# Kernel optimization log

Measured on AMD Instinct MI355X. Metric: run time of the kernel, lower is better.

The kernel has to match this reference:

```python
import jax, jax.numpy as jnp
import numpy as np

B, N, K, E, D, L, LM = 4, 5000, 4, 80000, 512, 6, 3
EPS_MSG = 1e-7   # GENConv message eps
EPS_SM = 1e-16   # PyG scatter-softmax eps
EPS_BN = 1e-5    # BatchNorm eps (eval: running mean=0, var=1)
EPS_LN = 1e-5


def setup_inputs() -> dict:
    key = jax.random.key(0)
    ks = jax.random.split(key, 12)
    s = 0.04  # weight scale for stability
    return {
        "x_idx": jax.random.randint(ks[0], (B, N, K), 0, 25, dtype=jnp.int32),
        "edge_index": jax.random.randint(ks[1], (2, E), 0, N, dtype=jnp.int32),
        "edge_weight": jax.random.uniform(ks[2], (E,), dtype=jnp.float32),
        "node_emb": jax.random.normal(ks[3], (25, D), dtype=jnp.float32),
        "W1": jax.random.normal(ks[4], (L, D, 2 * D), dtype=jnp.float32) * s,
        "b1": jnp.zeros((L, 2 * D), jnp.float32),
        "g1": jnp.ones((L, 2 * D), jnp.float32),
        "be1": jnp.zeros((L, 2 * D), jnp.float32),
        "W2": jax.random.normal(ks[5], (L, 2 * D, D), dtype=jnp.float32) * s,
        "b2": jnp.zeros((L, D), jnp.float32),
        "ln_g": jnp.ones((D,), jnp.float32),
        "ln_b": jnp.zeros((D,), jnp.float32),
        "Wm": jax.random.normal(ks[6], (LM, D, D), dtype=jnp.float32) * s,
        "bm": jnp.zeros((LM, D), jnp.float32),
        "Wout": jax.random.normal(ks[7], (D, 1), dtype=jnp.float32) * s,
        "bout": jnp.zeros((1,), jnp.float32),
    }


def _gen_conv(x, src, dst, edge_weight, W1, b1, g1, be1, W2, b2):
    # x: [B,N,D]; GENConv(aggr='softmax', t=1, num_layers=2, norm='batch' in eval)
    x_j = x[:, src, :]                                            # [B,E,D] gather
    msg = jax.nn.relu(x_j + edge_weight[None, :, None]) + EPS_MSG # [B,E,D]

    def seg_softmax_agg(m):  # m: [E,D] -> [N,D]
        mx = jax.ops.segment_max(m, dst, num_segments=N)          # [N,D]
        ex = jnp.exp(m - mx[dst])
        den = jax.ops.segment_sum(ex, dst, num_segments=N)
        alpha = ex / (den[dst] + EPS_SM)
        return jax.ops.segment_sum(m * alpha, dst, num_segments=N)

    agg = jax.vmap(seg_softmax_agg)(msg)                          # [B,N,D]
    out = agg + x                                                 # residual with x_dst
    h = out @ W1 + b1                                             # [B,N,2D]
    h = h / jnp.sqrt(1.0 + EPS_BN) * g1 + be1                     # BN eval (mean=0, var=1)
    h = jax.nn.relu(h)
    return h @ W2 + b2                                            # [B,N,D]


def reference(x_idx, edge_index, edge_weight, node_emb, W1, b1, g1, be1, W2, b2,
              ln_g, ln_b, Wm, bm, Wout, bout):
    src, dst = edge_index[0], edge_index[1]
    x = node_emb[x_idx].sum(axis=2)                               # [B,N,D]
    for l in range(W1.shape[0]):
        x = _gen_conv(x, src, dst, edge_weight,
                      W1[l], b1[l], g1[l], be1[l], W2[l], b2[l])
        x = jax.nn.relu(x)                                        # EncoderLayer relu (dropout=id in eval)
    mu = x.mean(axis=-1, keepdims=True)
    var = jnp.mean(jnp.square(x - mu), axis=-1, keepdims=True)
    h = (x - mu) * jax.lax.rsqrt(var + EPS_LN) * ln_g + ln_b      # LayerNorm
    for l in range(Wm.shape[0]):
        h = jax.nn.gelu(h @ Wm[l] + bm[l], approximate=False)
    out = h @ Wout + bout                                         # [B,N,1]
    return out.mean(axis=1)                                       # [B,1]
```

## Files before the change

kernel.cpp:

```cpp
#include <hip/hip_runtime.h>
#include <hip/hip_fp16.h>

#define BB 4
#define NN 5000
#define KK 4
#define EE 80000
#define DD 512
#define LL 6
#define LMM 3

typedef _Float16 f16x8 __attribute__((ext_vector_type(8)));
typedef _Float16 f16x4 __attribute__((ext_vector_type(4)));
typedef _Float16 f16x2 __attribute__((ext_vector_type(2)));
typedef float f32x4 __attribute__((ext_vector_type(4)));

__device__ __forceinline__ void async_copy16(_Float16* lds, const _Float16* g) {
    __builtin_amdgcn_global_load_lds((const __attribute__((address_space(1))) void*)g,
                                     (__attribute__((address_space(3))) void*)lds,
                                     16, 0, 0);
}

__global__ void zero_int2(int* a, int* b, int n) {
    int i = blockIdx.x * blockDim.x + threadIdx.x;
    if (i < n) { a[i] = 0; b[i] = 0; }
}

__global__ void count_deg(const int* __restrict__ dst, int* __restrict__ deg) {
    int e = blockIdx.x * blockDim.x + threadIdx.x;
    if (e < EE) atomicAdd(&deg[dst[e]], 1);
}

__global__ __launch_bounds__(1024) void scan_off(const int* __restrict__ deg, int* __restrict__ off) {
    __shared__ int s[1024];
    const int n = NN, tot = NN + 1;
    const int per = (tot + 1023) / 1024;
    int tid = threadIdx.x;
    int start = tid * per;
    int loc[8];
    int sum = 0;
    for (int i = 0; i < per; i++) {
        int idx = start + i;
        int v = (idx < n) ? deg[idx] : 0;
        loc[i] = sum; sum += v;
    }
    s[tid] = sum; __syncthreads();
    for (int o = 1; o < 1024; o <<= 1) {
        int v = (tid >= o) ? s[tid - o] : 0;
        __syncthreads();
        s[tid] += v;
        __syncthreads();
    }
    int base = (tid > 0) ? s[tid - 1] : 0;
    for (int i = 0; i < per; i++) {
        int idx = start + i;
        if (idx < tot) off[idx] = base + loc[i];
    }
}

__global__ void scatter_edges(const int* __restrict__ src, const int* __restrict__ dst,
                              const float* __restrict__ ew, const int* __restrict__ off,
                              int* __restrict__ cursor, int* __restrict__ srcs, float* __restrict__ wss) {
    int e = blockIdx.x * blockDim.x + threadIdx.x;
    if (e >= EE) return;
    int d = dst[e];
    int p = atomicAdd(&cursor[d], 1);
    int idx = off[d] + p;
    srcs[idx] = src[e];
    wss[idx] = ew[e];
}

__global__ __launch_bounds__(256) void embed_kernel(const int* __restrict__ x_idx,
                                                    const float* __restrict__ emb,
                                                    _Float16* __restrict__ x) {
    int row = blockIdx.x;
    int d = threadIdx.x * 2;
    int4 iv = *reinterpret_cast<const int4*>(x_idx + (size_t)row * 4);
    float2 a = *reinterpret_cast<const float2*>(emb + (size_t)iv.x * DD + d);
    float2 b = *reinterpret_cast<const float2*>(emb + (size_t)iv.y * DD + d);
    float2 c = *reinterpret_cast<const float2*>(emb + (size_t)iv.z * DD + d);
    float2 e = *reinterpret_cast<const float2*>(emb + (size_t)iv.w * DD + d);
    f16x2 v;
    v[0] = (_Float16)(a.x + b.x + c.x + e.x);
    v[1] = (_Float16)(a.y + b.y + c.y + e.y);
    *reinterpret_cast<f16x2*>(x + (size_t)row * DD + d) = v;
}

__global__ __launch_bounds__(128) void conv_kernel(const _Float16* __restrict__ x,
                                                   const int* __restrict__ srcs,
                                                   const float* __restrict__ wss,
                                                   const int* __restrict__ off,
                                                   _Float16* __restrict__ t) {
    int bh = blockIdx.x;
    int b = bh >> 1, h = bh & 1;
    int wave = threadIdx.x >> 6, lane = threadIdx.x & 63;
    int n = blockIdx.y * 2 + wave;
    const _Float16* xb = x + (size_t)b * NN * DD + h * (DD / 2);
    int e0 = off[n], e1 = off[n + 1];
    __shared__ int   ss[2][64];
    __shared__ float sw[2][64];
    int d0 = lane * 4;
    float S[4] = {0.f, 0.f, 0.f, 0.f};
    float Z[4] = {0.f, 0.f, 0.f, 0.f};
    for (int base = e0; base < e1; base += 64) {
        int cnt = min(64, e1 - base);
        if (lane < cnt) { ss[wave][lane] = srcs[base + lane]; sw[wave][lane] = wss[base + lane]; }
        for (int j = 0; j < cnt; j++) {
            f16x4 xv = *reinterpret_cast<const f16x4*>(xb + (size_t)ss[wave][j] * DD + d0);
            float w = sw[wave][j];
#pragma unroll
            for (int q = 0; q < 4; q++) {
                float m = fmaxf((float)xv[q] + w, 0.f);
                float p = __expf(m);
                S[q] += p;
                Z[q] = fmaf(m, p, Z[q]);
            }
        }
    }
    f16x4 xn = *reinterpret_cast<const f16x4*>(xb + (size_t)n * DD + d0);
    f16x4 o;
#pragma unroll
    for (int q = 0; q < 4; q++) {
        float agg = (e1 > e0) ? (Z[q] / (S[q] + 1e-16f) + 1e-7f) : 0.f;
        o[q] = (_Float16)(agg + (float)xn[q]);
    }
    *reinterpret_cast<f16x4*>(t + ((size_t)b * NN + n) * DD + h * (DD / 2) + d0) = o;
}

__global__ void transpose_f32_f16(const float* __restrict__ W, _Float16* __restrict__ Wt,
                                  int K, int Nc) {
    __shared__ float tile[32][33];
    size_t loff = (size_t)blockIdx.z * K * Nc;
    int n0 = blockIdx.x * 32, k0 = blockIdx.y * 32;
    int tx = threadIdx.x, ty = threadIdx.y;
    for (int i = 0; i < 32; i += 8)
        tile[ty + i][tx] = W[loff + (size_t)(k0 + ty + i) * Nc + n0 + tx];
    __syncthreads();
    for (int i = 0; i < 32; i += 8)
        Wt[loff + (size_t)(n0 + ty + i) * K + k0 + tx] = (_Float16)tile[tx][ty + i];
}

template <int MODE>
__global__ __launch_bounds__(256) void gemm_kernel(const _Float16* __restrict__ A,
                                                   const _Float16* __restrict__ Bt,
                                                   const float* __restrict__ bias,
                                                   const float* __restrict__ g,
                                                   const float* __restrict__ be,
                                                   _Float16* __restrict__ Cout,
                                                   int M, int N, int K, int nt) {
    constexpr int BM = 128, BN = 128, BK = 32;
    constexpr int BUF = (BM + BN) * BK;
    __shared__ __align__(16) _Float16 smem[2 * BUF];
    int tid = threadIdx.x;
    int bid = blockIdx.x;
    int xcd = bid & 7, gidx = bid >> 3;
    int m0 = (xcd + 8 * (gidx / nt)) * BM;
    int n0 = (gidx % nt) * BN;
    int lane = tid & 63, wave = tid >> 6;
    int wm = (wave & 1) * 64, wn = (wave >> 1) * 64;
    int l16 = lane & 15, quad = lane >> 4;
    int r0 = tid >> 2, r1 = r0 + 64;
    int c0s = ((tid & 3) ^ (r0 & 3)) * 8;
    int c1s = ((tid & 3) ^ (r1 & 3)) * 8;
    const _Float16* pa0 = A + (size_t)min(m0 + r0, M - 1) * K + c0s;
    const _Float16* pa1 = A + (size_t)min(m0 + r1, M - 1) * K + c1s;
    const _Float16* pb0 = Bt + (size_t)(n0 + r0) * K + c0s;
    const _Float16* pb1 = Bt + (size_t)(n0 + r1) * K + c1s;
    int la0 = tid * 8, la1 = (tid + 256) * 8;
    int lb0 = BM * BK + la0, lb1 = BM * BK + la1;

    f32x4 acc[4][4] = {};
    async_copy16(smem + la0, pa0);
    async_copy16(smem + la1, pa1);
    async_copy16(smem + lb0, pb0);
    async_copy16(smem + lb1, pb1);
    int buf = 0;
    int qa = (quad ^ (l16 & 3)) * 8;
    for (int k0 = 0; k0 < K; k0 += BK, buf ^= BUF) {
        __syncthreads();
        int kn = k0 + BK;
        int nb = buf ^ BUF;
        if (kn < K) {
            async_copy16(smem + nb + la0, pa0 + kn);
            async_copy16(smem + nb + la1, pa1 + kn);
            async_copy16(smem + nb + lb0, pb0 + kn);
            async_copy16(smem + nb + lb1, pb1 + kn);
        }
        f16x8 af[4], bf[4];
#pragma unroll
        for (int i = 0; i < 4; i++)
            af[i] = *reinterpret_cast<const f16x8*>(&smem[buf + (wm + i * 16 + l16) * BK + qa]);
#pragma unroll
        for (int j = 0; j < 4; j++)
            bf[j] = *reinterpret_cast<const f16x8*>(&smem[buf + BM * BK + (wn + j * 16 + l16) * BK + qa]);
#pragma unroll
        for (int i = 0; i < 4; i++)
#pragma unroll
            for (int j = 0; j < 4; j++)
                acc[i][j] = __builtin_amdgcn_mfma_f32_16x16x32_f16(af[i], bf[j], acc[i][j], 0, 0, 0);
    }
    __syncthreads();
    const float invs = rsqrtf(1.0f + 1e-5f);
    _Float16* Ct = smem;
#pragma unroll
    for (int p = 0; p < 2; p++) {
        if ((wave >> 1) == p) {
#pragma unroll
            for (int i = 0; i < 4; i++) {
#pragma unroll
                for (int j = 0; j < 4; j++) {
                    int col = n0 + wn + j * 16 + l16;
#pragma unroll
                    for (int r = 0; r < 4; r++) {
                        float v = acc[i][j][r] + bias[col];
                        if (MODE == 0) {
                            v = fmaxf(v * (g[col] * invs) + be[col], 0.f);
                        } else if (MODE == 1) {
                            v = fmaxf(v, 0.f);
                        } else {
                            v = 0.5f * v * (1.0f + erff(v * 0.70710678118654752f));
                        }
                        Ct[(wm + i * 16 + quad * 4 + r) * 64 + j * 16 + l16] = (_Float16)v;
                    }
                }
            }
        }
        __syncthreads();
#pragma unroll
        for (int k = 0; k < 4; k++) {
            int ch = tid + 256 * k;
            int row = ch >> 3, cc = (ch & 7) * 8;
            int grow = m0 + row;
            if (grow < M)
                *reinterpret_cast<f16x8*>(Cout + (size_t)grow * N + n0 + p * 64 + cc) =
                    *reinterpret_cast<const f16x8*>(&Ct[row * 64 + cc]);
        }
        __syncthreads();
    }
}

__device__ __forceinline__ float block_sum_256(float v, volatile float* sbuf) {
    __syncthreads();
    for (int s = 32; s; s >>= 1) v += __shfl_down(v, s);
    int wv = threadIdx.x >> 6, ln = threadIdx.x & 63;
    if (ln == 0) sbuf[wv] = v;
    __syncthreads();
    if (threadIdx.x == 0) sbuf[4] = sbuf[0] + sbuf[1] + sbuf[2] + sbuf[3];
    __syncthreads();
    return sbuf[4];
}

__global__ __launch_bounds__(256) void ln_kernel(const _Float16* __restrict__ x,
                                                 const float* __restrict__ lg,
                                                 const float* __restrict__ lb,
                                                 _Float16* __restrict__ t) {
    __shared__ float sbuf[5];
    size_t row = blockIdx.x;
    int d = threadIdx.x * 2;
    f16x2 xv = *reinterpret_cast<const f16x2*>(x + row * DD + d);
    float v0 = (float)xv[0], v1 = (float)xv[1];
    float mu = block_sum_256(v0 + v1, sbuf) * (1.0f / DD);
    float d0 = v0 - mu, d1 = v1 - mu;
    float var = block_sum_256(d0 * d0 + d1 * d1, sbuf) * (1.0f / DD);
    float rs = rsqrtf(var + 1e-5f);
    f16x2 o;
    o[0] = (_Float16)(d0 * rs * lg[d] + lb[d]);
    o[1] = (_Float16)(d1 * rs * lg[d + 1] + lb[d + 1]);
    *reinterpret_cast<f16x2*>(t + row * DD + d) = o;
}

__global__ void init_out(float* out, const float* __restrict__ bout) {
    if (threadIdx.x < BB) out[threadIdx.x] = bout[0];
}

__global__ __launch_bounds__(256) void final_reduce(const _Float16* __restrict__ h,
                                                    const float* __restrict__ wout,
                                                    float* __restrict__ out) {
    int b = blockIdx.y;
    const _Float16* hb = h + (size_t)b * NN * DD;
    int lane = threadIdx.x & 63, wave = threadIdx.x >> 6;
    float wv[8];
#pragma unroll
    for (int j = 0; j < 8; j++) wv[j] = wout[lane * 8 + j];
    float acc = 0.f;
    for (int n = blockIdx.x * 4 + wave; n < NN; n += gridDim.x * 4) {
        f16x8 hv = *reinterpret_cast<const f16x8*>(hb + (size_t)n * DD + lane * 8);
#pragma unroll
        for (int j = 0; j < 8; j++) acc += (float)hv[j] * wv[j];
    }
    for (int s = 32; s; s >>= 1) acc += __shfl_down(acc, s);
    __shared__ float sb[4];
    if (lane == 0) sb[wave] = acc;
    __syncthreads();
    if (threadIdx.x == 0) atomicAdd(&out[b], (sb[0] + sb[1] + sb[2] + sb[3]) * (1.0f / NN));
}

extern "C" void kernel_launch(void* const* d_in, const int* in_sizes, int n_in,
                              void* d_out, int out_size, void* d_ws, size_t ws_size,
                              hipStream_t stream) {
    const int*   x_idx = (const int*)d_in[0];
    const int*   eidx  = (const int*)d_in[1];
    const float* ew    = (const float*)d_in[2];
    const float* emb   = (const float*)d_in[3];
    const float* W1    = (const float*)d_in[4];
    const float* b1    = (const float*)d_in[5];
    const float* g1    = (const float*)d_in[6];
    const float* be1   = (const float*)d_in[7];
    const float* W2    = (const float*)d_in[8];
    const float* b2    = (const float*)d_in[9];
    const float* lng   = (const float*)d_in[10];
    const float* lnb   = (const float*)d_in[11];
    const float* Wm    = (const float*)d_in[12];
    const float* bm    = (const float*)d_in[13];
    const float* Wout  = (const float*)d_in[14];
    const float* bout  = (const float*)d_in[15];
    float* out = (float*)d_out;

    char* w = (char*)d_ws;
    size_t o = 0;
    auto alloc = [&](size_t bytes) -> void* {
        void* p = w + o;
        o = (o + bytes + 255) & ~(size_t)255;
        return p;
    };
    _Float16*  x    = (_Float16*)alloc((size_t)BB * NN * DD * 2);
    _Float16*  t    = (_Float16*)alloc((size_t)BB * NN * DD * 2);
    _Float16*  h    = (_Float16*)alloc((size_t)BB * NN * 2 * DD * 2);
    _Float16*  W1t  = (_Float16*)alloc((size_t)LL * 2 * DD * DD * 2);
    _Float16*  W2t  = (_Float16*)alloc((size_t)LL * DD * 2 * DD * 2);
    _Float16*  Wmt  = (_Float16*)alloc((size_t)LMM * DD * DD * 2);
    int*    deg    = (int*)alloc((size_t)NN * 4);
    int*    offs   = (int*)alloc((size_t)(NN + 1) * 4);
    int*    cursor = (int*)alloc((size_t)NN * 4);
    int*    srcs   = (int*)alloc((size_t)EE * 4);
    float*  wss    = (float*)alloc((size_t)EE * 4);

    const int* src = eidx;
    const int* dst = eidx + EE;

    zero_int2<<<(NN + 255) / 256, 256, 0, stream>>>(deg, cursor, NN);
    count_deg<<<(EE + 255) / 256, 256, 0, stream>>>(dst, deg);
    scan_off<<<1, 1024, 0, stream>>>(deg, offs);
    scatter_edges<<<(EE + 255) / 256, 256, 0, stream>>>(src, dst, ew, offs, cursor, srcs, wss);
    embed_kernel<<<BB * NN, 256, 0, stream>>>(x_idx, emb, x);

    transpose_f32_f16<<<dim3(2 * DD / 32, DD / 32, LL), dim3(32, 8), 0, stream>>>(W1, W1t, DD, 2 * DD);
    transpose_f32_f16<<<dim3(DD / 32, 2 * DD / 32, LL), dim3(32, 8), 0, stream>>>(W2, W2t, 2 * DD, DD);
    transpose_f32_f16<<<dim3(DD / 32, DD / 32, LMM), dim3(32, 8), 0, stream>>>(Wm, Wmt, DD, DD);

    const int M = BB * NN;
    const int mt8 = ((M + 127) / 128 + 7) & ~7;
    for (int l = 0; l < LL; l++) {
        conv_kernel<<<dim3(2 * BB, NN / 2), 128, 0, stream>>>(x, srcs, wss, offs, t);
        gemm_kernel<0><<<mt8 * 8, 256, 0, stream>>>(
            t, W1t + (size_t)l * 2 * DD * DD, b1 + (size_t)l * 2 * DD,
            g1 + (size_t)l * 2 * DD, be1 + (size_t)l * 2 * DD, h, M, 2 * DD, DD, 8);
        gemm_kernel<1><<<mt8 * 4, 256, 0, stream>>>(
            h, W2t + (size_t)l * DD * 2 * DD, b2 + (size_t)l * DD,
            nullptr, nullptr, x, M, DD, 2 * DD, 4);
    }
    ln_kernel<<<M, 256, 0, stream>>>(x, lng, lnb, t);
    gemm_kernel<2><<<mt8 * 4, 256, 0, stream>>>(
        t, Wmt, bm, nullptr, nullptr, h, M, DD, DD, 4);
    gemm_kernel<2><<<mt8 * 4, 256, 0, stream>>>(
        h, Wmt + (size_t)DD * DD, bm + DD, nullptr, nullptr, t, M, DD, DD, 4);
    gemm_kernel<2><<<mt8 * 4, 256, 0, stream>>>(
        t, Wmt + (size_t)2 * DD * DD, bm + 2 * DD, nullptr, nullptr, h, M, DD, DD, 4);
    init_out<<<1, 64, 0, stream>>>(out, bout);
    final_reduce<<<dim3(32, BB), 256, 0, stream>>>(h, Wout, out);
}
```

Baseline: 919.9 us.

## Process all batches per node in conv kernel and pack edge src/weight

```diff
diff --git a/kernel.cpp b/kernel.cpp
--- a/kernel.cpp
+++ b/kernel.cpp
@@ -59,14 +59,12 @@
 
 __global__ void scatter_edges(const int* __restrict__ src, const int* __restrict__ dst,
                               const float* __restrict__ ew, const int* __restrict__ off,
-                              int* __restrict__ cursor, int* __restrict__ srcs, float* __restrict__ wss) {
+                              int* __restrict__ cursor, int2* __restrict__ epk) {
     int e = blockIdx.x * blockDim.x + threadIdx.x;
     if (e >= EE) return;
     int d = dst[e];
     int p = atomicAdd(&cursor[d], 1);
-    int idx = off[d] + p;
-    srcs[idx] = src[e];
-    wss[idx] = ew[e];
+    epk[off[d] + p] = make_int2(src[e], __float_as_int(ew[e]));
 }
 
 __global__ __launch_bounds__(256) void embed_kernel(const int* __restrict__ x_idx,
@@ -86,44 +84,45 @@
 }
 
 __global__ __launch_bounds__(128) void conv_kernel(const _Float16* __restrict__ x,
-                                                   const int* __restrict__ srcs,
-                                                   const float* __restrict__ wss,
+                                                   const int2* __restrict__ epk,
                                                    const int* __restrict__ off,
                                                    _Float16* __restrict__ t) {
-    int bh = blockIdx.x;
-    int b = bh >> 1, h = bh & 1;
+    int n = blockIdx.x;
     int wave = threadIdx.x >> 6, lane = threadIdx.x & 63;
-    int n = blockIdx.y * 2 + wave;
-    const _Float16* xb = x + (size_t)b * NN * DD + h * (DD / 2);
     int e0 = off[n], e1 = off[n + 1];
-    __shared__ int   ss[2][64];
-    __shared__ float sw[2][64];
-    int d0 = lane * 4;
-    float S[4] = {0.f, 0.f, 0.f, 0.f};
-    float Z[4] = {0.f, 0.f, 0.f, 0.f};
-    for (int base = e0; base < e1; base += 64) {
-        int cnt = min(64, e1 - base);
-        if (lane < cnt) { ss[wave][lane] = srcs[base + lane]; sw[wave][lane] = wss[base + lane]; }
-        for (int j = 0; j < cnt; j++) {
-            f16x4 xv = *reinterpret_cast<const f16x4*>(xb + (size_t)ss[wave][j] * DD + d0);
-            float w = sw[wave][j];
+    int vo = wave * (DD / 2) + lane * 4;
+    const int2* ep = epk + e0;
+    int num = e1 - e0;
+    float S[16], Z[16];
+#pragma unroll
+    for (int q = 0; q < 16; q++) { S[q] = 0.f; Z[q] = 0.f; }
+    for (int j = 0; j < num; j++) {
+        int2 e = ep[j];
+        int sj = e.x;
+        float w = __int_as_float(e.y);
+#pragma unroll
+        for (int b = 0; b < 4; b++) {
+            f16x4 xv = *reinterpret_cast<const f16x4*>(x + ((size_t)b * NN + sj) * DD + vo);
 #pragma unroll
             for (int q = 0; q < 4; q++) {
                 float m = fmaxf((float)xv[q] + w, 0.f);
                 float p = __expf(m);
-                S[q] += p;
-                Z[q] = fmaf(m, p, Z[q]);
+                S[b * 4 + q] += p;
+                Z[b * 4 + q] = fmaf(m, p, Z[b * 4 + q]);
             }
         }
     }
-    f16x4 xn = *reinterpret_cast<const f16x4*>(xb + (size_t)n * DD + d0);
-    f16x4 o;
-#pragma unroll
-    for (int q = 0; q < 4; q++) {
-        float agg = (e1 > e0) ? (Z[q] / (S[q] + 1e-16f) + 1e-7f) : 0.f;
-        o[q] = (_Float16)(agg + (float)xn[q]);
-    }
-    *reinterpret_cast<f16x4*>(t + ((size_t)b * NN + n) * DD + h * (DD / 2) + d0) = o;
+#pragma unroll
+    for (int b = 0; b < 4; b++) {
+        f16x4 xn = *reinterpret_cast<const f16x4*>(x + ((size_t)b * NN + n) * DD + vo);
+        f16x4 o;
+#pragma unroll
+        for (int q = 0; q < 4; q++) {
+            float agg = (num > 0) ? (Z[b * 4 + q] / (S[b * 4 + q] + 1e-16f) + 1e-7f) : 0.f;
+            o[q] = (_Float16)(agg + (float)xn[q]);
+        }
+        *reinterpret_cast<f16x4*>(t + ((size_t)b * NN + n) * DD + vo) = o;
+    }
 }
 
 __global__ void transpose_f32_f16(const float* __restrict__ W, _Float16* __restrict__ Wt,
@@ -331,8 +330,7 @@
     int*    deg    = (int*)alloc((size_t)NN * 4);
     int*    offs   = (int*)alloc((size_t)(NN + 1) * 4);
     int*    cursor = (int*)alloc((size_t)NN * 4);
-    int*    srcs   = (int*)alloc((size_t)EE * 4);
-    float*  wss    = (float*)alloc((size_t)EE * 4);
+    int2*   epk    = (int2*)alloc((size_t)EE * 8);
 
     const int* src = eidx;
     const int* dst = eidx + EE;
@@ -340,7 +338,7 @@
     zero_int2<<<(NN + 255) / 256, 256, 0, stream>>>(deg, cursor, NN);
     count_deg<<<(EE + 255) / 256, 256, 0, stream>>>(dst, deg);
     scan_off<<<1, 1024, 0, stream>>>(deg, offs);
-    scatter_edges<<<(EE + 255) / 256, 256, 0, stream>>>(src, dst, ew, offs, cursor, srcs, wss);
+    scatter_edges<<<(EE + 255) / 256, 256, 0, stream>>>(src, dst, ew, offs, cursor, epk);
     embed_kernel<<<BB * NN, 256, 0, stream>>>(x_idx, emb, x);
 
     transpose_f32_f16<<<dim3(2 * DD / 32, DD / 32, LL), dim3(32, 8), 0, stream>>>(W1, W1t, DD, 2 * DD);
@@ -350,7 +348,7 @@
     const int M = BB * NN;
     const int mt8 = ((M + 127) / 128 + 7) & ~7;
     for (int l = 0; l < LL; l++) {
-        conv_kernel<<<dim3(2 * BB, NN / 2), 128, 0, stream>>>(x, srcs, wss, offs, t);
+        conv_kernel<<<NN, 128, 0, stream>>>(x, epk, offs, t);
         gemm_kernel<0><<<mt8 * 8, 256, 0, stream>>>(
             t, W1t + (size_t)l * 2 * DD * DD, b1 + (size_t)l * 2 * DD,
             g1 + (size_t)l * 2 * DD, be1 + (size_t)l * 2 * DD, h, M, 2 * DD, DD, 8);
```

Measured after the change: 990.4 us. 7.7% more time.
